# Performance work log

Hardware: AMD Instinct MI355X
Metric: run time of the kernel (lower is better)

## Reference

```python
import jax, jax.numpy as jnp
import numpy as np

D_MODEL = 2048
D_FF = 8192
EPS = 1e-5


def layernorm(x, g, b):
    m = x.mean(-1, keepdims=True)
    v = ((x - m) ** 2).mean(-1, keepdims=True)
    return (x - m) * jax.lax.rsqrt(v + EPS) * g + b


def rotate_half(x):
    return jnp.concatenate([-x[..., ::2], x[..., 1::2]], axis=-1)


def sinu_pos_emb(dim, length):
    inv_freq = 1.0 / 10000 ** (jnp.arange(0, dim, 2, dtype=jnp.float32) / dim)
    pos = jnp.arange(length, dtype=jnp.float32)
    sp = pos[:, None] * inv_freq[None, :]           # [S, dim/2]
    return jnp.concatenate([jnp.sin(sp), jnp.cos(sp)], axis=-1)  # [S, dim]


def setup_inputs() -> dict:
    key = jax.random.key(0)
    ks = jax.random.split(key, 10)
    d, f = D_MODEL, D_FF
    sc = 0.02
    return {
        "src":  jax.random.normal(ks[0], (4, 2048, d), jnp.float32),
        "Wqkv": jax.random.normal(ks[1], (3 * d, d), jnp.float32) * sc,
        "bqkv": jnp.zeros((3 * d,), jnp.float32),
        "Wo":   jax.random.normal(ks[2], (d, d), jnp.float32) * sc,
        "bo":   jnp.zeros((d,), jnp.float32),
        "W1":   jax.random.normal(ks[3], (f, d), jnp.float32) * sc,
        "b1":   jnp.zeros((f,), jnp.float32),
        "W2":   jax.random.normal(ks[4], (d, f), jnp.float32) * sc,
        "b2":   jnp.zeros((d,), jnp.float32),
        "g1":   jnp.ones((d,), jnp.float32),
        "be1":  jnp.zeros((d,), jnp.float32),
        "g2":   jnp.ones((d,), jnp.float32),
        "be2":  jnp.zeros((d,), jnp.float32),
    }


def reference(src, Wqkv, bqkv, Wo, bo, W1, b1, W2, b2, g1, be1, g2, be2):
    B, S, d = src.shape
    # norm1 (note: torch code reassigns src, so residuals use the normed value)
    src = layernorm(src, g1, be1)
    qkv = src @ Wqkv.T + bqkv                      # [B,S,3d]
    Q, K, V = qkv[..., :d], qkv[..., d:2 * d], qkv[..., 2 * d:]
    # rotary: cos/sin of the (sin,cos)-concatenated table, faithful to source
    emb = sinu_pos_emb(d, S)                       # [S,d]
    c, s = jnp.cos(emb), jnp.sin(emb)
    Q = Q * c + rotate_half(Q) * s
    K = K * c - rotate_half(K) * s
    # causal SDPA over full d_model (no head split in source)
    scale = 1.0 / jnp.sqrt(jnp.float32(d))
    scores = jnp.einsum('bqd,bkd->bqk', Q, K) * scale
    causal = jnp.tril(jnp.ones((S, S), bool))
    scores = jnp.where(causal, scores, jnp.float32(-1e30))
    P = jax.nn.softmax(scores, axis=-1)
    attn = jnp.einsum('bqk,bkd->bqd', P, V)
    src = src + attn @ Wo.T + bo
    # FFN block
    h = layernorm(src, g2, be2)
    h = jax.nn.relu(h @ W1.T + b1) @ W2.T + b2
    return src + h
```

## Files before the change

kernel.cpp:

```cpp
#include <hip/hip_runtime.h>
#include <cstdint>


typedef __attribute__((ext_vector_type(8))) short short8;
typedef __attribute__((ext_vector_type(4))) float floatx4;

#define PLANE 16777216L
#define SS    4194304L

__device__ __forceinline__ float bf2f(unsigned short u) {
    union { unsigned int i; float f; } v; v.i = ((unsigned int)u) << 16; return v.f;
}
__device__ __forceinline__ unsigned short f2bf(float f) {
    union { float f; unsigned int i; } v; v.f = f;
    unsigned int x = v.i;
    return (unsigned short)((x + 0x7FFFu + ((x >> 16) & 1u)) >> 16);
}
__device__ __forceinline__ uint4 pack8(float4 a, float4 b) {
    unsigned short o[8];
    o[0] = f2bf(a.x); o[1] = f2bf(a.y); o[2] = f2bf(a.z); o[3] = f2bf(a.w);
    o[4] = f2bf(b.x); o[5] = f2bf(b.y); o[6] = f2bf(b.z); o[7] = f2bf(b.w);
    return *(uint4*)o;
}
__device__ __forceinline__ void gl_lds16(const void* g, void* l) {
    __builtin_amdgcn_global_load_lds(
        (const __attribute__((address_space(1))) void*)g,
        (__attribute__((address_space(3))) void*)l, 16, 0, 0);
}

#define EM_QKV  0
#define EM_SC   1
#define EM_PV   2
#define EM_PROJ 3
#define EM_FFN1 4
#define EM_F2A  5

template<int EM>
__launch_bounds__(256, 2)
__global__ void gemm_bt(const unsigned short* __restrict__ A,
                        const unsigned short* __restrict__ B,
                        void* __restrict__ Cv, int N, int K,
                        const float* __restrict__ bias,
                        const unsigned short* __restrict__ resid16,
                        unsigned short* __restrict__ outQ,
                        unsigned short* __restrict__ outVt)
{
    constexpr int BM = 128, BN = 128, BK = 32;
    __shared__ __align__(16) unsigned short As[BM * BK];
    __shared__ __align__(16) unsigned short Bs[BN * BK];

    const int m0 = blockIdx.x * BM, n0 = blockIdx.y * BN;
    if (EM == EM_SC && n0 > m0 + (BM - 1)) return;

    int kmax = K;
    if (EM == EM_PV) { kmax = m0 + BM; if (kmax > K) kmax = K; }
    const int nsteps = kmax / BK;

    const int t = threadIdx.x;
    const int lane = t & 63, wave = t >> 6;
    const int q = lane >> 4, ln = lane & 15;
    const int wm = (wave >> 1) * 64, wn = (wave & 1) * 64;

    const int r0 = wave * 32;
    const int rA = r0 + (lane >> 2);
    const int cslot = lane & 3;
    const int cg0 = (cslot ^ (rA & 3)) * 8;
    const int cg1 = (cslot ^ ((rA + 16) & 3)) * 8;
    const unsigned short* Agp0 = A + (long)(m0 + rA) * K + cg0;
    const unsigned short* Agp1 = A + (long)(m0 + rA + 16) * K + cg1;
    const unsigned short* Bgp0 = B + (long)(n0 + rA) * K + cg0;
    const unsigned short* Bgp1 = B + (long)(n0 + rA + 16) * K + cg1;
    unsigned short* lA0 = &As[r0 * 32];
    unsigned short* lA1 = &As[(r0 + 16) * 32];
    unsigned short* lB0 = &Bs[r0 * 32];
    unsigned short* lB1 = &Bs[(r0 + 16) * 32];

    floatx4 acc[4][4];
#pragma unroll
    for (int i = 0; i < 4; ++i)
#pragma unroll
        for (int j = 0; j < 4; ++j) acc[i][j] = (floatx4){0.f, 0.f, 0.f, 0.f};

    for (int s = 0; s < nsteps; ++s) {
        const long off = (long)s * BK;
        __syncthreads();
        gl_lds16(Agp0 + off, lA0);
        gl_lds16(Agp1 + off, lA1);
        gl_lds16(Bgp0 + off, lB0);
        gl_lds16(Bgp1 + off, lB1);
        __syncthreads();
        short8 af[4], bfr[4];
#pragma unroll
        for (int i = 0; i < 4; ++i) {
            const int R = wm + 16 * i + ln;
            af[i] = *(const short8*)&As[R * 32 + ((q ^ (R & 3)) * 8)];
        }
#pragma unroll
        for (int j = 0; j < 4; ++j) {
            const int R = wn + 16 * j + ln;
            bfr[j] = *(const short8*)&Bs[R * 32 + ((q ^ (R & 3)) * 8)];
        }
#pragma unroll
        for (int i = 0; i < 4; ++i)
#pragma unroll
            for (int j = 0; j < 4; ++j)
                acc[i][j] = __builtin_amdgcn_mfma_f32_16x16x32_bf16(af[i], bfr[j], acc[i][j], 0, 0, 0);
    }

#pragma unroll
    for (int i = 0; i < 4; ++i) {
#pragma unroll
        for (int r = 0; r < 4; ++r) {
            const int row = m0 + wm + 16 * i + q * 4 + r;
#pragma unroll
            for (int j = 0; j < 4; ++j) {
                const int col = n0 + wn + 16 * j + ln;
                float v = acc[i][j][r];
                const long idx = (long)row * N + col;
                if constexpr (EM == EM_SC) {
                    ((unsigned short*)Cv)[idx] = f2bf(v);
                } else if constexpr (EM == EM_PV) {
                    ((unsigned short*)Cv)[idx] = f2bf(v);
                }
            }
        }
    }
}

#define BARM()   do { __builtin_amdgcn_s_barrier(); asm volatile("" ::: "memory"); } while (0)
#define LGKM0()  asm volatile("s_waitcnt lgkmcnt(0)" ::: "memory")
#define VMCNT(n) asm volatile("s_waitcnt vmcnt(" #n ")" ::: "memory")
#define SCHEDB() __builtin_amdgcn_sched_barrier(0)
#define PRIO1()  __builtin_amdgcn_s_setprio(1)
#define PRIO0()  __builtin_amdgcn_s_setprio(0)

template<int EM>
__launch_bounds__(512, 2)
__global__ void gemm256(const unsigned short* __restrict__ A,
                        const unsigned short* __restrict__ B,
                        void* __restrict__ Cv, int N, int K,
                        const float* __restrict__ bias,
                        const unsigned short* __restrict__ resid16,
                        unsigned short* __restrict__ outQ,
                        unsigned short* __restrict__ outVt)
{
    __shared__ __align__(16) unsigned short As[2][16384];
    __shared__ __align__(16) unsigned short Bs[2][16384];

    const int m0 = blockIdx.x * 256, n0 = blockIdx.y * 256;
    const int t = threadIdx.x;
    const int lane = t & 63, wave = t >> 6;
    const int q = lane >> 4, ln = lane & 15;
    const int wm = wave >> 2, wn = wave & 3;

    const int srow = t >> 3;
    const int csrcS = ((t & 7) ^ (srow & 7)) * 8;
    const unsigned short* AgS = A + (long)(m0 + srow) * K + csrcS;
    const unsigned short* BgS = B + (long)(n0 + srow) * K + csrcS;
    const int wslice = wave * 512;

    const int aBase = (wm * 128 + ln) * 64;
    const int bBase = (wn * 64 + ln) * 64;
    const int c0 = ((0 + q) ^ (ln & 7)) * 8;
    const int c1 = ((4 + q) ^ (ln & 7)) * 8;

    floatx4 acc[8][4];
#pragma unroll
    for (int i = 0; i < 8; ++i)
#pragma unroll
        for (int j = 0; j < 4; ++j) acc[i][j] = (floatx4){0.f, 0.f, 0.f, 0.f};

    short8 a[4][2];
    short8 b0r[2][2], b1r[2][2];

#define STAGE_A(buf, kt, h) do { \
    const unsigned short* _g = AgS + (long)((h) * 128) * K + ((long)(kt) << 6); \
    gl_lds16(_g,           &As[buf][(h) * 8192 + wslice]); \
    gl_lds16(_g + 64L * K, &As[buf][(h) * 8192 + 4096 + wslice]); \
} while (0)
#define STAGE_B(buf, kt, h) do { \
    const unsigned short* _g = BgS + (long)((h) * 128) * K + ((long)(kt) << 6); \
    gl_lds16(_g,           &Bs[buf][(h) * 8192 + wslice]); \
    gl_lds16(_g + 64L * K, &Bs[buf][(h) * 8192 + 4096 + wslice]); \
} while (0)
#define RD_A(sel, mg) { \
    _Pragma("unroll") \
    for (int i = 0; i < 4; ++i) { \
        a[i][0] = *(const short8*)&As[sel][aBase + ((mg) * 64 + 16 * i) * 64 + c0]; \
        a[i][1] = *(const short8*)&As[sel][aBase + ((mg) * 64 + 16 * i) * 64 + c1]; \
    } }
#define RD_B0(sel) { \
    _Pragma("unroll") \
    for (int j = 0; j < 2; ++j) { \
        b0r[j][0] = *(const short8*)&Bs[sel][bBase + (16 * j) * 64 + c0]; \
        b0r[j][1] = *(const short8*)&Bs[sel][bBase + (16 * j) * 64 + c1]; } }
#define RD_B1(sel) { \
    _Pragma("unroll") \
    for (int j = 0; j < 2; ++j) { \
        b1r[j][0] = *(const short8*)&Bs[sel][bBase + (32 + 16 * j) * 64 + c0]; \
        b1r[j][1] = *(const short8*)&Bs[sel][bBase + (32 + 16 * j) * 64 + c1]; } }
#define MMQ(mg, br, ng) { \
    _Pragma("unroll") \
    for (int i = 0; i < 4; ++i) \
    _Pragma("unroll") \
    for (int j = 0; j < 2; ++j) { \
        acc[(mg)*4+i][(ng)*2+j] = __builtin_amdgcn_mfma_f32_16x16x32_bf16( \
            a[i][0], br[j][0], acc[(mg)*4+i][(ng)*2+j], 0, 0, 0); \
        acc[(mg)*4+i][(ng)*2+j] = __builtin_amdgcn_mfma_f32_16x16x32_bf16( \
            a[i][1], br[j][1], acc[(mg)*4+i][(ng)*2+j], 0, 0, 0); \
    } }

    const int NG = K >> 6;

    STAGE_A(0, 0, 0); STAGE_A(0, 0, 1);
    STAGE_B(0, 0, 0); STAGE_B(0, 0, 1);
    STAGE_A(1, 1, 0);
    VMCNT(2); BARM();

    for (int g = 0; g < NG - 2; ++g) {
        const int cur = g & 1, nxt = cur ^ 1;
        STAGE_A(nxt, g + 1, 1);
        RD_A(cur, 0); RD_B0(cur);
        BARM(); LGKM0(); SCHEDB();
        PRIO1(); MMQ(0, b0r, 0); PRIO0();
        BARM();
        STAGE_B(nxt, g + 1, 0);
        RD_B1(cur);
        BARM(); LGKM0(); SCHEDB();
        PRIO1(); MMQ(0, b1r, 1); PRIO0();
        BARM();
        STAGE_B(nxt, g + 1, 1);
        RD_A(cur, 1);
        BARM(); LGKM0(); SCHEDB();
        PRIO1(); MMQ(1, b0r, 0); PRIO0();
        BARM();
        STAGE_A(cur, g + 2, 0);
        BARM(); SCHEDB();
        PRIO1(); MMQ(1, b1r, 1); PRIO0();
        VMCNT(2); BARM();
    }
    {
        const int g = NG - 2, cur = g & 1, nxt = cur ^ 1;
        STAGE_A(nxt, g + 1, 1);
        RD_A(cur, 0); RD_B0(cur);
        BARM(); LGKM0(); SCHEDB();
        PRIO1(); MMQ(0, b0r, 0); PRIO0();
        BARM();
        STAGE_B(nxt, g + 1, 0);
        RD_B1(cur);
        BARM(); LGKM0(); SCHEDB();
        PRIO1(); MMQ(0, b1r, 1); PRIO0();
        BARM();
        STAGE_B(nxt, g + 1, 1);
        RD_A(cur, 1);
        BARM(); LGKM0(); SCHEDB();
        PRIO1(); MMQ(1, b0r, 0); PRIO0();
        BARM();
        SCHEDB();
        PRIO1(); MMQ(1, b1r, 1); PRIO0();
        VMCNT(0); BARM();
    }
    {
        const int cur = (NG - 1) & 1;
        RD_A(cur, 0); RD_B0(cur);
        LGKM0(); SCHEDB();
        PRIO1(); MMQ(0, b0r, 0); PRIO0();
        RD_B1(cur);
        LGKM0(); SCHEDB();
        PRIO1(); MMQ(0, b1r, 1); PRIO0();
        RD_A(cur, 1);
        LGKM0(); SCHEDB();
        PRIO1(); MMQ(1, b0r, 0); PRIO0();
        PRIO1(); MMQ(1, b1r, 1); PRIO0();
    }

#undef STAGE_A
#undef STAGE_B
#undef RD_A
#undef RD_B0
#undef RD_B1
#undef MMQ

#pragma unroll
    for (int i = 0; i < 8; ++i) {
#pragma unroll
        for (int r = 0; r < 4; ++r) {
            const int row = m0 + wm * 128 + 16 * i + q * 4 + r;
#pragma unroll
            for (int j = 0; j < 4; ++j) {
                const int col = n0 + wn * 64 + 16 * j + ln;
                float v = acc[i][j][r];
                const long idx = (long)row * N + col;
                if constexpr (EM == EM_QKV) {
                    v += bias[col];
                    const unsigned short vb = f2bf(v);
                    const int p = col >> 11, c2 = col & 2047;
                    if (p == 0)      outQ[(long)row * 2048 + c2] = vb;
                    else if (p == 1) (outQ + PLANE)[(long)row * 2048 + c2] = vb;
                    else             outVt[(long)(row >> 11) * SS + (long)c2 * 2048 + (row & 2047)] = vb;
                } else if constexpr (EM == EM_PROJ) {
                    v += bias[col] + bf2f(resid16[idx]);
                    ((float*)Cv)[idx] = v;
                } else if constexpr (EM == EM_FFN1) {
                    v = fmaxf(v + bias[col], 0.f);
                    ((unsigned short*)Cv)[idx] = f2bf(v);
                } else {
                    ((float*)Cv)[idx] += v;
                }
            }
        }
    }
}

__launch_bounds__(256)
__global__ void cvt_rows(const float* __restrict__ src, unsigned short* __restrict__ dst, long srcld)
{
    const int row = blockIdx.x, t = threadIdx.x;
    const float* s = src + (long)row * srcld + t * 8;
    float4 a = *(const float4*)s;
    float4 b = *(const float4*)(s + 4);
    *(uint4*)(dst + (long)row * 2048 + t * 8) = pack8(a, b);
}

__launch_bounds__(256)
__global__ void layernorm_k(const float* __restrict__ X, unsigned short* __restrict__ Y,
                            const float* __restrict__ g, const float* __restrict__ be)
{
    const int row = blockIdx.x, t = threadIdx.x;
    const float* Xr = X + (long)row * 2048 + t * 8;
    float4 v0 = *(const float4*)Xr;
    float4 v1 = *(const float4*)(Xr + 4);
    float x[8] = {v0.x, v0.y, v0.z, v0.w, v1.x, v1.y, v1.z, v1.w};
    float s = 0.f, ss = 0.f;
#pragma unroll
    for (int k = 0; k < 8; ++k) { s += x[k]; ss += x[k] * x[k]; }
    for (int off = 32; off; off >>= 1) { s += __shfl_down(s, off, 64); ss += __shfl_down(ss, off, 64); }
    __shared__ float red[8];
    const int wave = t >> 6, lane = t & 63;
    if (lane == 0) { red[wave] = s; red[4 + wave] = ss; }
    __syncthreads();
    s  = red[0] + red[1] + red[2] + red[3];
    ss = red[4] + red[5] + red[6] + red[7];
    const float mean = s * (1.f / 2048.f);
    const float var  = ss * (1.f / 2048.f) - mean * mean;
    const float rstd = rsqrtf(var + 1e-5f);
    unsigned short o[8];
#pragma unroll
    for (int k = 0; k < 8; ++k) {
        const int col = t * 8 + k;
        o[k] = f2bf((x[k] - mean) * rstd * g[col] + be[col]);
    }
    *(uint4*)(Y + (long)row * 2048 + t * 8) = *(uint4*)o;
}

__launch_bounds__(256)
__global__ void rope_inplace(unsigned short* __restrict__ Q, unsigned short* __restrict__ K)
{
    __shared__ __align__(16) unsigned short rowbuf[2048];
    const int row = blockIdx.x;
    const int mtx = blockIdx.y;
    unsigned short* X = (mtx ? K : Q) + (long)row * 2048;
    const int t = threadIdx.x;
    *(uint4*)&rowbuf[t * 8] = *(const uint4*)(X + t * 8);
    __syncthreads();
    const int p = row & 2047;
    const float sgn = mtx ? -1.f : 1.f;
    unsigned short o[8];
#pragma unroll
    for (int e = 0; e < 8; ++e) {
        const int j = t * 8 + e;
        const int i = j & 1023;
        const float freq = __expf(-(float)i * (9.210340371976184f / 1024.0f));
        const float sp = (float)p * freq;
        const float emb = (j < 1024) ? sinf(sp) : cosf(sp);
        float se, ce;
        sincosf(emb, &se, &ce);
        const int pj = (j < 1024) ? (2 * j) : (2 * j - 2047);
        float xp = bf2f(rowbuf[pj]);
        if (j < 1024) xp = -xp;
        o[e] = f2bf(bf2f(rowbuf[j]) * ce + sgn * xp * se);
    }
    *(uint4*)(X + t * 8) = *(uint4*)o;
}

__launch_bounds__(256)
__global__ void softmax_causal(unsigned short* __restrict__ S)
{
    const int qq = blockIdx.x;
    const int L = qq + 1;
    unsigned short* srow = S + (long)qq * 2048;
    const int t = threadIdx.x;
    const float scale = 0.022097086912079608f;
    float vals[8];
    float m = -1e30f;
#pragma unroll
    for (int u = 0; u < 8; ++u) {
        const int i2 = t + 256 * u;
        vals[u] = (i2 < L) ? bf2f(srow[i2]) * scale : -1e30f;
        m = fmaxf(m, vals[u]);
    }
    for (int off = 32; off; off >>= 1) m = fmaxf(m, __shfl_down(m, off, 64));
    __shared__ float red[8];
    const int wave = t >> 6, lane = t & 63;
    if (lane == 0) red[wave] = m;
    __syncthreads();
    m = fmaxf(fmaxf(red[0], red[1]), fmaxf(red[2], red[3]));
    float sum = 0.f;
#pragma unroll
    for (int u = 0; u < 8; ++u) {
        float e = __expf(vals[u] - m);
        e = (t + 256 * u < L) ? e : 0.f;
        vals[u] = e; sum += e;
    }
    for (int off = 32; off; off >>= 1) sum += __shfl_down(sum, off, 64);
    if (lane == 0) red[4 + wave] = sum;
    __syncthreads();
    sum = red[4] + red[5] + red[6] + red[7];
    const float inv = 1.0f / sum;
#pragma unroll
    for (int u = 0; u < 8; ++u) srow[t + 256 * u] = f2bf(vals[u] * inv);
}

__launch_bounds__(256)
__global__ void final_add(float* __restrict__ io, const float* __restrict__ b2)
{
    const int row = blockIdx.x, t = threadIdx.x;
    const long base = (long)row * 2048 + t * 8;
    float4 a0 = *(const float4*)(io + base);
    float4 a1 = *(const float4*)(io + base + 4);
    float4 c0 = *(const float4*)(b2 + t * 8);
    float4 c1 = *(const float4*)(b2 + t * 8 + 4);
    a0.x += c0.x; a0.y += c0.y; a0.z += c0.z; a0.w += c0.w;
    a1.x += c1.x; a1.y += c1.y; a1.z += c1.z; a1.w += c1.w;
    *(float4*)(io + base) = a0;
    *(float4*)(io + base + 4) = a1;
}

extern "C" void kernel_launch(void* const* d_in, const int* in_sizes, int n_in,
                              void* d_out, int out_size, void* d_ws, size_t ws_size,
                              hipStream_t stream)
{
    const float* src  = (const float*)d_in[0];
    const float* Wqkv = (const float*)d_in[1];
    const float* bqkv = (const float*)d_in[2];
    const float* Wo   = (const float*)d_in[3];
    const float* bo   = (const float*)d_in[4];
    const float* W1   = (const float*)d_in[5];
    const float* b1   = (const float*)d_in[6];
    const float* W2   = (const float*)d_in[7];
    const float* b2   = (const float*)d_in[8];
    const float* g1   = (const float*)d_in[9];
    const float* be1  = (const float*)d_in[10];
    const float* g2   = (const float*)d_in[11];
    const float* be2  = (const float*)d_in[12];

    char* ws = (char*)d_ws;
    const long MB = 1LL << 20;
    unsigned short* x1    = (unsigned short*)ws;
    unsigned short* Vt    = (unsigned short*)(ws + 32 * MB);
    unsigned short* Wqbf  = (unsigned short*)(ws + 64 * MB);
    unsigned short* attn  = (unsigned short*)(ws + 64 * MB);
    unsigned short* scP   = (unsigned short*)(ws + 96 * MB);
    unsigned short* Wobf  = (unsigned short*)(ws + 96 * MB);
    unsigned short* W1c   = (unsigned short*)(ws + 96 * MB);
    unsigned short* W2c   = (unsigned short*)(ws + 104 * MB);
    unsigned short* h2    = x1;
    unsigned short* f1    = Vt;

    unsigned short* Q    = (unsigned short*)d_out;
    float*          src2 = (float*)d_out;
    float*          out  = (float*)d_out;

    const dim3 blk(256);
    const dim3 blk512(512);

    cvt_rows<<<6144, blk, 0, stream>>>(Wqkv, Wqbf, 2048);
    layernorm_k<<<8192, blk, 0, stream>>>(src, x1, g1, be1);
    gemm256<EM_QKV><<<dim3(32, 24), blk512, 0, stream>>>(
        x1, Wqbf, nullptr, 6144, 2048, bqkv, nullptr, Q, Vt);
    rope_inplace<<<dim3(8192, 2), blk, 0, stream>>>(Q, Q + PLANE);

    for (int b = 0; b < 4; ++b) {
        gemm_bt<EM_SC><<<dim3(16, 16), blk, 0, stream>>>(
            Q + b * SS, Q + PLANE + b * SS, scP, 2048, 2048, nullptr, nullptr, nullptr, nullptr);
        softmax_causal<<<2048, blk, 0, stream>>>(scP);
        gemm_bt<EM_PV><<<dim3(16, 16), blk, 0, stream>>>(
            scP, Vt + b * SS, attn + b * SS, 2048, 2048, nullptr, nullptr, nullptr, nullptr);
    }

    cvt_rows<<<2048, blk, 0, stream>>>(Wo, Wobf, 2048);
    gemm256<EM_PROJ><<<dim3(32, 8), blk512, 0, stream>>>(
        attn, Wobf, src2, 2048, 2048, bo, x1, nullptr, nullptr);
    layernorm_k<<<8192, blk, 0, stream>>>(src2, h2, g2, be2);

    for (int c = 0; c < 4; ++c) {
        cvt_rows<<<2048, blk, 0, stream>>>(W1 + (long)c * 2048 * 2048, W1c, 2048);
        cvt_rows<<<2048, blk, 0, stream>>>(W2 + (long)c * 2048, W2c, 8192);
        gemm256<EM_FFN1><<<dim3(32, 8), blk512, 0, stream>>>(
            h2, W1c, f1, 2048, 2048, b1 + c * 2048, nullptr, nullptr, nullptr);
        gemm256<EM_F2A><<<dim3(32, 8), blk512, 0, stream>>>(
            f1, W2c, src2, 2048, 2048, nullptr, nullptr, nullptr, nullptr);
    }
    final_add<<<8192, blk, 0, stream>>>(out, b2);
}
```

Baseline: 1.674 ms.

## Shrink gemm256 to 256x128 tiles with K=32 steps and XCD-aware block remap

Restructures the main bf16 GEMM from 512-thread 256x256 tiles with 64-wide K steps to 256-thread 256x128 tiles with 32-wide K steps. LDS shrinks accordingly, the grids double, and a block-index remap groups consecutive workgroups across the eight XCDs. The aim is more resident blocks and better tail balance and cache locality. In exchange each block loads more operand data per flop and runs twice as many barrier-heavy K iterations. The epilogue, not shown, must stay consistent with the new wave layout.

Measured after the change: 1.895 ms. +13.2%, slower.

```diff
diff --git a/kernel.cpp b/kernel.cpp
--- a/kernel.cpp
+++ b/kernel.cpp
@@ -135,7 +135,7 @@
 #define PRIO0()  __builtin_amdgcn_s_setprio(0)
 
 template<int EM>
-__launch_bounds__(512, 2)
+__launch_bounds__(256, 2)
 __global__ void gemm256(const unsigned short* __restrict__ A,
                         const unsigned short* __restrict__ B,
                         void* __restrict__ Cv, int N, int K,
@@ -144,25 +144,29 @@
                         unsigned short* __restrict__ outQ,
                         unsigned short* __restrict__ outVt)
 {
-    __shared__ __align__(16) unsigned short As[2][16384];
-    __shared__ __align__(16) unsigned short Bs[2][16384];
-
-    const int m0 = blockIdx.x * 256, n0 = blockIdx.y * 256;
+    __shared__ __align__(16) unsigned short As[2][8192];
+    __shared__ __align__(16) unsigned short Bs[2][4096];
+
+    const int nwg = gridDim.x * gridDim.y;
+    int wg = blockIdx.y * gridDim.x + blockIdx.x;
+    wg = (wg & 7) * (nwg >> 3) + (wg >> 3);
+    const int m0 = (wg % gridDim.x) * 256;
+    const int n0 = (wg / gridDim.x) * 128;
+
     const int t = threadIdx.x;
     const int lane = t & 63, wave = t >> 6;
     const int q = lane >> 4, ln = lane & 15;
-    const int wm = wave >> 2, wn = wave & 3;
-
-    const int srow = t >> 3;
-    const int csrcS = ((t & 7) ^ (srow & 7)) * 8;
+    const int wm = wave >> 1, wn = wave & 1;
+
+    const int srow = t >> 2;
+    const int csrcS = ((t & 3) ^ (srow & 3)) * 8;
     const unsigned short* AgS = A + (long)(m0 + srow) * K + csrcS;
     const unsigned short* BgS = B + (long)(n0 + srow) * K + csrcS;
-    const int wslice = wave * 512;
-
-    const int aBase = (wm * 128 + ln) * 64;
-    const int bBase = (wn * 64 + ln) * 64;
-    const int c0 = ((0 + q) ^ (ln & 7)) * 8;
-    const int c1 = ((4 + q) ^ (ln & 7)) * 8;
+    const int wv512 = wave * 512;
+
+    const int aBase = (wm * 128 + ln) * 32;
+    const int bBase = (wn * 64 + ln) * 32;
+    const int cR = ((q ^ (ln & 3)) * 8);
 
     floatx4 acc[8][4];
 #pragma unroll
@@ -170,47 +174,37 @@
 #pragma unroll
         for (int j = 0; j < 4; ++j) acc[i][j] = (floatx4){0.f, 0.f, 0.f, 0.f};
 
-    short8 a[4][2];
-    short8 b0r[2][2], b1r[2][2];
+    short8 a[4];
+    short8 b0r[2], b1r[2];
 
 #define STAGE_A(buf, kt, h) do { \
-    const unsigned short* _g = AgS + (long)((h) * 128) * K + ((long)(kt) << 6); \
-    gl_lds16(_g,           &As[buf][(h) * 8192 + wslice]); \
-    gl_lds16(_g + 64L * K, &As[buf][(h) * 8192 + 4096 + wslice]); \
+    const unsigned short* _g = AgS + (long)((h) * 128) * K + ((long)(kt) << 5); \
+    gl_lds16(_g,           &As[buf][(h) * 4096 + wv512]); \
+    gl_lds16(_g + 64L * K, &As[buf][(h) * 4096 + 2048 + wv512]); \
 } while (0)
 #define STAGE_B(buf, kt, h) do { \
-    const unsigned short* _g = BgS + (long)((h) * 128) * K + ((long)(kt) << 6); \
-    gl_lds16(_g,           &Bs[buf][(h) * 8192 + wslice]); \
-    gl_lds16(_g + 64L * K, &Bs[buf][(h) * 8192 + 4096 + wslice]); \
+    const unsigned short* _g = BgS + (long)((h) * 64) * K + ((long)(kt) << 5); \
+    gl_lds16(_g, &Bs[buf][(h) * 2048 + wv512]); \
 } while (0)
 #define RD_A(sel, mg) { \
     _Pragma("unroll") \
-    for (int i = 0; i < 4; ++i) { \
-        a[i][0] = *(const short8*)&As[sel][aBase + ((mg) * 64 + 16 * i) * 64 + c0]; \
-        a[i][1] = *(const short8*)&As[sel][aBase + ((mg) * 64 + 16 * i) * 64 + c1]; \
-    } }
+    for (int i = 0; i < 4; ++i) \
+        a[i] = *(const short8*)&As[sel][aBase + ((mg) * 64 + 16 * i) * 32 + cR]; }
 #define RD_B0(sel) { \
-    _Pragma("unroll") \
-    for (int j = 0; j < 2; ++j) { \
-        b0r[j][0] = *(const short8*)&Bs[sel][bBase + (16 * j) * 64 + c0]; \
-        b0r[j][1] = *(const short8*)&Bs[sel][bBase + (16 * j) * 64 + c1]; } }
+    b0r[0] = *(const short8*)&Bs[sel][bBase + 0 * 32 + cR]; \
+    b0r[1] = *(const short8*)&Bs[sel][bBase + 16 * 32 + cR]; }
 #define RD_B1(sel) { \
-    _Pragma("unroll") \
-    for (int j = 0; j < 2; ++j) { \
-        b1r[j][0] = *(const short8*)&Bs[sel][bBase + (32 + 16 * j) * 64 + c0]; \
-        b1r[j][1] = *(const short8*)&Bs[sel][bBase + (32 + 16 * j) * 64 + c1]; } }
+    b1r[0] = *(const short8*)&Bs[sel][bBase + 32 * 32 + cR]; \
+    b1r[1] = *(const short8*)&Bs[sel][bBase + 48 * 32 + cR]; }
 #define MMQ(mg, br, ng) { \
     _Pragma("unroll") \
     for (int i = 0; i < 4; ++i) \
     _Pragma("unroll") \
-    for (int j = 0; j < 2; ++j) { \
+    for (int j = 0; j < 2; ++j) \
         acc[(mg)*4+i][(ng)*2+j] = __builtin_amdgcn_mfma_f32_16x16x32_bf16( \
-            a[i][0], br[j][0], acc[(mg)*4+i][(ng)*2+j], 0, 0, 0); \
-        acc[(mg)*4+i][(ng)*2+j] = __builtin_amdgcn_mfma_f32_16x16x32_bf16( \
-            a[i][1], br[j][1], acc[(mg)*4+i][(ng)*2+j], 0, 0, 0); \
-    } }
-
-    const int NG = K >> 6;
+            a[i], br[j], acc[(mg)*4+i][(ng)*2+j], 0, 0, 0); }
+
+    const int NG = K >> 5;
 
     STAGE_A(0, 0, 0); STAGE_A(0, 0, 1);
     STAGE_B(0, 0, 0); STAGE_B(0, 0, 1);
@@ -224,12 +218,11 @@
         BARM(); LGKM0(); SCHEDB();
         PRIO1(); MMQ(0, b0r, 0); PRIO0();
         BARM();
-        STAGE_B(nxt, g + 1, 0);
+        STAGE_B(nxt, g + 1, 0); STAGE_B(nxt, g + 1, 1);
         RD_B1(cur);
         BARM(); LGKM0(); SCHEDB();
         PRIO1(); MMQ(0, b1r, 1); PRIO0();
         BARM();
-        STAGE_B(nxt, g + 1, 1);
         RD_A(cur, 1);
         BARM(); LGKM0(); SCHEDB();
         PRIO1(); MMQ(1, b0r, 0); PRIO0();
@@ -246,12 +239,11 @@
         BARM(); LGKM0(); SCHEDB();
         PRIO1(); MMQ(0, b0r, 0); PRIO0();
         BARM();
-        STAGE_B(nxt, g + 1, 0);
+        STAGE_B(nxt, g + 1, 0); STAGE_B(nxt, g + 1, 1);
         RD_B1(cur);
         BARM(); LGKM0(); SCHEDB();
         PRIO1(); MMQ(0, b1r, 1); PRIO0();
         BARM();
-        STAGE_B(nxt, g + 1, 1);
         RD_A(cur, 1);
         BARM(); LGKM0(); SCHEDB();
         PRIO1(); MMQ(1, b0r, 0); PRIO0();
@@ -472,11 +464,10 @@
     float*          out  = (float*)d_out;
 
     const dim3 blk(256);
-    const dim3 blk512(512);
 
     cvt_rows<<<6144, blk, 0, stream>>>(Wqkv, Wqbf, 2048);
     layernorm_k<<<8192, blk, 0, stream>>>(src, x1, g1, be1);
-    gemm256<EM_QKV><<<dim3(32, 24), blk512, 0, stream>>>(
+    gemm256<EM_QKV><<<dim3(32, 48), blk, 0, stream>>>(
         x1, Wqbf, nullptr, 6144, 2048, bqkv, nullptr, Q, Vt);
     rope_inplace<<<dim3(8192, 2), blk, 0, stream>>>(Q, Q + PLANE);
 
@@ -489,16 +480,16 @@
     }
 
     cvt_rows<<<2048, blk, 0, stream>>>(Wo, Wobf, 2048);
-    gemm256<EM_PROJ><<<dim3(32, 8), blk512, 0, stream>>>(
+    gemm256<EM_PROJ><<<dim3(32, 16), blk, 0, stream>>>(
         attn, Wobf, src2, 2048, 2048, bo, x1, nullptr, nullptr);
     layernorm_k<<<8192, blk, 0, stream>>>(src2, h2, g2, be2);
 
     for (int c = 0; c < 4; ++c) {
         cvt_rows<<<2048, blk, 0, stream>>>(W1 + (long)c * 2048 * 2048, W1c, 2048);
         cvt_rows<<<2048, blk, 0, stream>>>(W2 + (long)c * 2048, W2c, 8192);
-        gemm256<EM_FFN1><<<dim3(32, 8), blk512, 0, stream>>>(
+        gemm256<EM_FFN1><<<dim3(32, 16), blk, 0, stream>>>(
             h2, W1c, f1, 2048, 2048, b1 + c * 2048, nullptr, nullptr, nullptr);
-        gemm256<EM_F2A><<<dim3(32, 8), blk512, 0, stream>>>(
+        gemm256<EM_F2A><<<dim3(32, 16), blk, 0, stream>>>(
             f1, W2c, src2, 2048, 2048, nullptr, nullptr, nullptr, nullptr);
     }
     final_add<<<8192, blk, 0, stream>>>(out, b2);
```
